# Performance work log

Hardware: AMD Instinct MI355X
Metric: run time of the kernel (lower is better)

## Reference

```python
import jax, jax.numpy as jnp
import numpy as np
from jax import lax

NUM_HEADS = 8
EPS = 1e-12  # torch F.normalize default eps


def setup_inputs() -> dict:
    key = jax.random.key(0)
    ks = jax.random.split(key, 7)
    B, C, H, W = 4, 128, 256, 256
    d = C // 2  # per-branch channels = 64
    x = jax.random.normal(ks[0], (B, C, H, W), jnp.float32)
    w_qkv1 = jax.random.normal(ks[1], (3 * d, d), jnp.float32) * 0.05
    w_qkv2 = jax.random.normal(ks[2], (3 * d, d), jnp.float32) * 0.05
    w_dw1 = jax.random.normal(ks[3], (3 * d, 1, 3, 3), jnp.float32) * 0.05
    w_dw2 = jax.random.normal(ks[4], (3 * d, 1, 3, 3), jnp.float32) * 0.05
    w_po1 = jax.random.normal(ks[5], (d, d), jnp.float32) * 0.05
    w_po2 = jax.random.normal(ks[6], (d, d), jnp.float32) * 0.05
    t1 = jnp.ones((NUM_HEADS, 1, 1), jnp.float32)
    t2 = jnp.ones((NUM_HEADS, 1, 1), jnp.float32)
    return {"x": x, "w_qkv1": w_qkv1, "w_qkv2": w_qkv2, "w_dw1": w_dw1,
            "w_dw2": w_dw2, "w_po1": w_po1, "w_po2": w_po2, "t1": t1, "t2": t2}


def _qkv(xb, w1x1, wdw):
    # 1x1 conv (pointwise) then 3x3 depthwise conv, no bias
    y = jnp.einsum('bchw,oc->bohw', xb, w1x1)
    y = lax.conv_general_dilated(
        y, wdw, window_strides=(1, 1), padding='SAME',
        dimension_numbers=('NCHW', 'OIHW', 'NCHW'),
        feature_group_count=y.shape[1])
    return y


def _heads(t, b, h, w):
    # b (head c) h w -> b head c (h*w)
    return t.reshape(b, NUM_HEADS, -1, h * w)


def _l2norm(t):
    n = jnp.sqrt(jnp.sum(t * t, axis=-1, keepdims=True))
    return t / jnp.maximum(n, EPS)


def reference(x, w_qkv1, w_qkv2, w_dw1, w_dw2, w_po1, w_po2, t1, t2):
    b, c, h, w = x.shape
    x1, x2 = jnp.split(x, 2, axis=1)
    q1, k1, v1 = jnp.split(_qkv(x1, w_qkv1, w_dw1), 3, axis=1)
    q2, k2, v2 = jnp.split(_qkv(x2, w_qkv2, w_dw2), 3, axis=1)
    q1, k1, v1 = (_heads(t, b, h, w) for t in (q1, k1, v1))
    q2, k2, v2 = (_heads(t, b, h, w) for t in (q2, k2, v2))
    q1, k1 = _l2norm(q1), _l2norm(k1)
    q2, k2 = _l2norm(q2), _l2norm(k2)
    # channel-wise attention: [b, head, c_h, c_h]
    attn1 = jax.nn.softmax(jnp.einsum('bhcn,bhdn->bhcd', q1, k1) * t1[None], axis=-1)
    attn2 = jax.nn.softmax(jnp.einsum('bhcn,bhdn->bhcd', q2, k2) * t2[None], axis=-1)
    # cross-branch V swap
    out1 = jnp.einsum('bhcd,bhdn->bhcn', attn1, v2).reshape(b, c // 2, h, w)
    out2 = jnp.einsum('bhcd,bhdn->bhcn', attn2, v1).reshape(b, c // 2, h, w)
    out1 = jnp.einsum('bchw,oc->bohw', out1, w_po1)
    out2 = jnp.einsum('bchw,oc->bohw', out2, w_po2)
    return jnp.concatenate([out1, out2], axis=1)
```

## Files before the change

### kernel.cpp

```cpp
#include <hip/hip_runtime.h>
#include <hip/hip_fp16.h>

#define NPIX 65536
#define WIMG 256
#define HIMG 256
#define TW 16
#define TH 8
#define HSTR 24
#define NSLOT 240
#define YCH 248

typedef __attribute__((ext_vector_type(8))) _Float16 half8;
typedef __attribute__((ext_vector_type(4))) float f32x4;

__device__ __forceinline__ unsigned int h2u(__half2 h) {
  union { __half2 h; unsigned int u; } c; c.h = h; return c.u;
}
__device__ __forceinline__ __half2 u2h(unsigned int u) {
  union { unsigned int u; __half2 h; } c; c.u = u; return c.h;
}
__device__ __forceinline__ __half2 sp2(_Float16 s) {
  union { _Float16 h[2]; __half2 v; } u; u.h[0] = s; u.h[1] = s; return u.v;
}
__device__ __forceinline__ int qk_idx(int ch, int pxblk) {
  return ch * 128 + ((pxblk ^ (ch & 7)) << 3);
}
__device__ __forceinline__ void ld16_lds(const void* g, void* l) {
  __builtin_amdgcn_global_load_lds(
      (const __attribute__((address_space(1))) unsigned int*)g,
      (__attribute__((address_space(3))) unsigned int*)l, 16, 0, 0);
}

__global__ __launch_bounds__(256)
void k_prep(const float* __restrict__ wq1, const float* __restrict__ wq2,
            const float* __restrict__ wd1, const float* __restrict__ wd2,
            float* __restrict__ zbuf,
            _Float16* __restrict__ wqh, _Float16* __restrict__ wdh) {
  int i = blockIdx.x * 256 + threadIdx.x;
  if (i < 6144) {
    zbuf[i] = 0.0f;
  } else {
    int j = i - 6144;
    if (j < 24576) {
      int br = j / 12288, r = j - br * 12288;
      wqh[j] = (_Float16)((br ? wq2 : wq1)[r]);
    } else {
      int k = j - 24576;
      int br = k / 3072, r = k - br * 3072;
      int o = r >> 4, t = r & 15;
      wdh[k] = (t < 9) ? (_Float16)((br ? wd2 : wd1)[o * 9 + t]) : (_Float16)0.0f;
    }
  }
}

__global__ __launch_bounds__(256)
void k_xt(const float* __restrict__ x, __half* __restrict__ xT) {
  __shared__ _Float16 tile[64 * 257];
  const int strip = blockIdx.x;
  const int br = blockIdx.y, b = blockIdx.z;
  const int tid = threadIdx.x;
  const float* xb = x + ((size_t)b * 128 + br * 64) * NPIX + strip * 256;
  #pragma unroll 8
  for (int c = 0; c < 64; ++c)
    tile[c * 257 + tid] = (_Float16)xb[(size_t)c * NPIX + tid];
  __syncthreads();
  __half* xo = xT + ((size_t)(b * 2 + br) * NPIX + strip * 256) * 64;
  const int j = tid & 7;
  #pragma unroll
  for (int i = 0; i < 8; ++i) {
    int p = (tid >> 3) + i * 32;
    half8 h;
    #pragma unroll
    for (int k = 0; k < 8; ++k) h[k] = tile[(j * 8 + k) * 257 + p];
    *(half8*)((_Float16*)xo + p * 64 + j * 8) = h;
  }
}

__global__ __launch_bounds__(256, 3)
void k_qkv(const __half* __restrict__ xT,
           const _Float16* __restrict__ wqh, const _Float16* __restrict__ wdh,
           const float* __restrict__ zpage,
           __half* __restrict__ vbuf, float* __restrict__ gram,
           float* __restrict__ sqq, float* __restrict__ sqk)
{
  __shared__ __align__(16) _Float16 xs[256 * 64];
  __shared__ __align__(16) _Float16 ys[32 * YCH];

  const int tid = threadIdx.x;
  const int lane = tid & 63;
  const int wid = tid >> 6;
  const int tile = blockIdx.x;
  const int br = blockIdx.y;
  const int b = blockIdx.z;
  const int tx0 = (tile & 15) * TW;
  const int ty0 = (tile >> 4) * TH;

  const _Float16* wqb = wqh + br * 12288;
  const _Float16* wdb = wdh + br * 3072;
  const __half* xTimg = xT + (size_t)(b * 2 + br) * NPIX * 64;

  {
    const int j = lane & 7, pl = lane >> 3;
    for (int it = wid; it < 30; it += 4) {
      int s = it * 8;
      int slot = s + pl;
      int hy = slot / HSTR;
      int hx = slot - hy * HSTR;
      int gy = ty0 - 1 + hy, gx = tx0 - 1 + hx;
      bool valid = (hx < 18) && ((unsigned)gy < HIMG) && ((unsigned)gx < WIMG);
      const void* src = valid
        ? (const void*)((const _Float16*)xTimg + (size_t)(gy * WIMG + gx) * 64
                        + ((j ^ (slot & 7)) << 3))
        : (const void*)((const char*)zpage + lane * 16);
      ld16_lds(src, (void*)(xs + s * 64));
    }
  }
  asm volatile("s_waitcnt vmcnt(0)" ::: "memory");
  __syncthreads();

  const int col = lane & 15;
  const int qrow = lane >> 4;
  const int oo = tid >> 3;
  const int row = tid & 7;

  unsigned int qreg[2][8], kreg[2][8];

  #pragma unroll
  for (int p = 0; p < 3; ++p) {
    #pragma unroll
    for (int h = 0; h < 2; ++h) {
      half8 wf[2][2];
      #pragma unroll
      for (int nt = 0; nt < 2; ++nt)
        #pragma unroll
        for (int kc = 0; kc < 2; ++kc)
          wf[kc][nt] = *(const half8*)(wqb
              + (((p * 64 + h * 32 + nt * 16 + col) << 6) + kc * 32 + qrow * 8));

      for (int mt = wid; mt < 15; mt += 4) {
        int px = mt * 16 + col;
        half8 af0 = *(const half8*)(xs + px * 64 + (((qrow    ) ^ (px & 7)) << 3));
        half8 af1 = *(const half8*)(xs + px * 64 + (((4 + qrow) ^ (px & 7)) << 3));
        f32x4 a0 = {0,0,0,0}, a1 = {0,0,0,0};
        a0 = __builtin_amdgcn_mfma_f32_16x16x32_f16(af0, wf[0][0], a0, 0, 0, 0);
        a0 = __builtin_amdgcn_mfma_f32_16x16x32_f16(af1, wf[1][0], a0, 0, 0, 0);
        a1 = __builtin_amdgcn_mfma_f32_16x16x32_f16(af0, wf[0][1], a1, 0, 0, 0);
        a1 = __builtin_amdgcn_mfma_f32_16x16x32_f16(af1, wf[1][1], a1, 0, 0, 0);
        int pxd = mt * 16 + qrow * 4;
        __half2* d0 = (__half2*)(ys + (col     ) * YCH + pxd);
        __half2* d1 = (__half2*)(ys + (col + 16) * YCH + pxd);
        d0[0] = __floats2half2_rn(a0[0], a0[1]);
        d0[1] = __floats2half2_rn(a0[2], a0[3]);
        d1[0] = __floats2half2_rn(a1[0], a1[1]);
        d1[1] = __floats2half2_rn(a1[2], a1[3]);
      }
      __syncthreads();

      {
        const int o = h * 32 + oo;
        const _Float16* wdp = wdb + ((p * 64 + o) << 4);
        half8 wv = *(const half8*)wdp;
        _Float16 w8v = wdp[8];
        __half2 w2[9];
        #pragma unroll
        for (int j = 0; j < 8; ++j) w2[j] = sp2(wv[j]);
        w2[8] = sp2(w8v);
        __half2 a[8];
        #pragma unroll
        for (int k2 = 0; k2 < 8; ++k2) a[k2] = u2h(0u);
        #pragma unroll
        for (int ky = 0; ky < 3; ++ky) {
          const _Float16* rp = ys + oo * YCH + (row + ky) * HSTR;
          uint4 ra = *(const uint4*)rp;
          uint4 rb = *(const uint4*)(rp + 8);
          unsigned int rc = *(const unsigned int*)(rp + 16);
          unsigned int A[9] = {ra.x, ra.y, ra.z, ra.w, rb.x, rb.y, rb.z, rb.w, rc};
          #pragma unroll
          for (int k2 = 0; k2 < 8; ++k2) {
            unsigned int M = (A[k2] >> 16) | (A[k2 + 1] << 16);
            a[k2] = __hfma2(w2[ky * 3 + 0], u2h(A[k2]), a[k2]);
            a[k2] = __hfma2(w2[ky * 3 + 1], u2h(M), a[k2]);
            a[k2] = __hfma2(w2[ky * 3 + 2], u2h(A[k2 + 1]), a[k2]);
          }
        }
        if (p == 0) {
          #pragma unroll
          for (int k2 = 0; k2 < 8; ++k2) qreg[h][k2] = h2u(a[k2]);
        } else if (p == 1) {
          #pragma unroll
          for (int k2 = 0; k2 < 8; ++k2) kreg[h][k2] = h2u(a[k2]);
        } else {
          __half* vrow = (__half*)(vbuf
              + ((size_t)((br * 4 + b) * 64 + o)) * NPIX
              + (ty0 + row) * WIMG + tx0);
          uint4 s0 = {h2u(a[0]), h2u(a[1]), h2u(a[2]), h2u(a[3])};
          uint4 s1 = {h2u(a[4]), h2u(a[5]), h2u(a[6]), h2u(a[7])};
          *(uint4*)vrow = s0;
          *(uint4*)(vrow + 8) = s1;
          if (h == 1) {
            _Float16* qsb = xs;
            _Float16* ksb = xs + 64 * 128;
            #pragma unroll
            for (int hh = 0; hh < 2; ++hh) {
              int ch = hh * 32 + oo;
              uint4 q0 = {qreg[hh][0], qreg[hh][1], qreg[hh][2], qreg[hh][3]};
              uint4 q1 = {qreg[hh][4], qreg[hh][5], qreg[hh][6], qreg[hh][7]};
              uint4 k0 = {kreg[hh][0], kreg[hh][1], kreg[hh][2], kreg[hh][3]};
              uint4 k1 = {kreg[hh][4], kreg[hh][5], kreg[hh][6], kreg[hh][7]};
              *(uint4*)(qsb + qk_idx(ch, 2 * row))     = q0;
              *(uint4*)(qsb + qk_idx(ch, 2 * row + 1)) = q1;
              *(uint4*)(ksb + qk_idx(ch, 2 * row))     = k0;
              *(uint4*)(ksb + qk_idx(ch, 2 * row + 1)) = k1;
            }
          }
        }
      }
      __syncthreads();
    }
  }

  {
    const _Float16* qsb = xs;
    const _Float16* ksb = xs + 64 * 128;
    f32x4 gqk = {0,0,0,0}, gqq = {0,0,0,0}, gkk = {0,0,0,0};
    int ch = wid * 16 + col;
    #pragma unroll
    for (int kc = 0; kc < 4; ++kc) {
      int pb = kc * 4 + qrow;
      half8 aq = *(const half8*)(qsb + qk_idx(ch, pb));
      half8 bk = *(const half8*)(ksb + qk_idx(ch, pb));
      gqk = __builtin_amdgcn_mfma_f32_16x16x32_f16(aq, bk, gqk, 0, 0, 0);
      gqq = __builtin_amdgcn_mfma_f32_16x16x32_f16(aq, aq, gqq, 0, 0, 0);
      gkk = __builtin_amdgcn_mfma_f32_16x16x32_f16(bk, bk, gkk, 0, 0, 0);
    }
    const int gb_off = (br * 4 + b);
    if (((lane >> 3) & 1) == (lane >> 5)) {
      float* gb = gram + gb_off * 512;
      int kch = ch;
      int qc0 = wid * 16 + qrow * 4;
      #pragma unroll
      for (int r = 0; r < 4; ++r) {
        int qch = qc0 + r;
        atomicAdd(&gb[(qch >> 3) * 64 + (qch & 7) * 8 + (kch & 7)], gqk[r]);
      }
    }
    if ((col >> 2) == qrow) {
      atomicAdd(&sqq[gb_off * 64 + ch], gqq[lane & 3]);
      atomicAdd(&sqk[gb_off * 64 + ch], gkk[lane & 3]);
    }
  }
}

__global__ __launch_bounds__(64)
void k_attn(const float* __restrict__ gram, const float* __restrict__ sqq,
            const float* __restrict__ sqk,
            const float* __restrict__ wpo1, const float* __restrict__ wpo2,
            const float* __restrict__ t1, const float* __restrict__ t2,
            _Float16* __restrict__ wefft)
{
  const int br = blockIdx.x, b = blockIdx.y;
  const int t = threadIdx.x;
  __shared__ float attn[8][8][8];
  const float* gb = gram + (br * 4 + b) * 512;
  const float* sq = sqq + (br * 4 + b) * 64;
  const float* sk = sqk + (br * 4 + b) * 64;
  const float* tt = br ? t2 : t1;
  {
    int h = t >> 3, cq = t & 7;
    float ts = tt[h];
    float qn = fmaxf(sqrtf(sq[h * 8 + cq]), 1e-12f);
    float lg[8], m = -1e30f;
    #pragma unroll
    for (int d2 = 0; d2 < 8; ++d2) {
      float kn = fmaxf(sqrtf(sk[h * 8 + d2]), 1e-12f);
      lg[d2] = ts * gb[h * 64 + cq * 8 + d2] / (qn * kn);
      m = fmaxf(m, lg[d2]);
    }
    float s = 0.f;
    #pragma unroll
    for (int d2 = 0; d2 < 8; ++d2) { lg[d2] = expf(lg[d2] - m); s += lg[d2]; }
    float inv = 1.0f / s;
    #pragma unroll
    for (int d2 = 0; d2 < 8; ++d2) attn[h][cq][d2] = lg[d2] * inv;
  }
  __syncthreads();
  const float* wpo = br ? wpo2 : wpo1;
  _Float16* wt = wefft + (br * 4 + b) * 4096;
  for (int cp = 0; cp < 64; ++cp) {
    int hp = cp >> 3, ip = cp & 7;
    float acc = 0.f;
    #pragma unroll
    for (int j = 0; j < 8; ++j)
      acc += wpo[t * 64 + hp * 8 + j] * attn[hp][j][ip];
    wt[t * 64 + cp] = (_Float16)acc;
  }
}

__global__ __launch_bounds__(256)
void k_out(const __half* __restrict__ vbuf, const _Float16* __restrict__ wefft,
           float* __restrict__ out)
{
  __shared__ __align__(16) _Float16 vs[64 * 128];
  __shared__ __align__(16) _Float16 vt[128 * 64];

  const int strip = blockIdx.x;
  const int obr = blockIdx.y, b = blockIdx.z;
  const int brv = 1 - obr;
  const int tid = threadIdx.x;
  const int lane = tid & 63;
  const int wid = tid >> 6;
  const int col = lane & 15;
  const int qrow = lane >> 4;

  const __half* vb = vbuf + ((size_t)(brv * 4 + b) * 64) * NPIX + strip * 128;

  for (int i = 0; i < 4; ++i) {
    int it = wid * 4 + i;
    const void* src = (const void*)((const _Float16*)vb
        + (size_t)(it * 4 + (lane >> 4)) * NPIX + (lane & 15) * 8);
    ld16_lds(src, (void*)(vs + it * 512));
  }
  asm volatile("s_waitcnt vmcnt(0)" ::: "memory");
  __syncthreads();

  {
    int px = tid & 127, cb = tid >> 7;
    #pragma unroll
    for (int j = 0; j < 4; ++j) {
      half8 h;
      #pragma unroll
      for (int e = 0; e < 8; ++e) h[e] = vs[(cb * 32 + j * 8 + e) * 128 + px];
      int chunk = cb * 4 + j;
      *(half8*)(vt + ((px * 8 + (chunk ^ (px & 7))) << 3)) = h;
    }
  }
  __syncthreads();

  const _Float16* wt = wefft + (obr * 4 + b) * 4096;
  half8 bf[2][4];
  #pragma unroll
  for (int nt = 0; nt < 4; ++nt)
    #pragma unroll
    for (int kc = 0; kc < 2; ++kc)
      bf[kc][nt] = *(const half8*)(wt + (nt * 16 + col) * 64 + kc * 32 + qrow * 8);

  float* ob = out + ((size_t)b * 128 + obr * 64) * NPIX + strip * 128;
  #pragma unroll
  for (int mi = 0; mi < 2; ++mi) {
    int mt = wid * 2 + mi;
    int px = mt * 16 + col;
    half8 af0 = *(const half8*)(vt + ((px * 8 + ((qrow    ) ^ (px & 7))) << 3));
    half8 af1 = *(const half8*)(vt + ((px * 8 + ((4 + qrow) ^ (px & 7))) << 3));
    f32x4 acc[4] = {{0,0,0,0},{0,0,0,0},{0,0,0,0},{0,0,0,0}};
    #pragma unroll
    for (int nt = 0; nt < 4; ++nt) {
      acc[nt] = __builtin_amdgcn_mfma_f32_16x16x32_f16(af0, bf[0][nt], acc[nt], 0, 0, 0);
      acc[nt] = __builtin_amdgcn_mfma_f32_16x16x32_f16(af1, bf[1][nt], acc[nt], 0, 0, 0);
    }
    int pxd = mt * 16 + qrow * 4;
    #pragma unroll
    for (int nt = 0; nt < 4; ++nt) {
      float4 s = {acc[nt][0], acc[nt][1], acc[nt][2], acc[nt][3]};
      *(float4*)(ob + (size_t)(nt * 16 + col) * NPIX + pxd) = s;
    }
  }
}

extern "C" void kernel_launch(void* const* d_in, const int* in_sizes, int n_in,
                              void* d_out, int out_size, void* d_ws, size_t ws_size,
                              hipStream_t stream) {
  const float* x     = (const float*)d_in[0];
  const float* wqkv1 = (const float*)d_in[1];
  const float* wqkv2 = (const float*)d_in[2];
  const float* wdw1  = (const float*)d_in[3];
  const float* wdw2  = (const float*)d_in[4];
  const float* wpo1  = (const float*)d_in[5];
  const float* wpo2  = (const float*)d_in[6];
  const float* t1    = (const float*)d_in[7];
  const float* t2    = (const float*)d_in[8];

  char* ws = (char*)d_ws;
  __half* vbuf = (__half*)ws;
  float* gram  = (float*)(ws + 67108864);
  float* sqq   = gram + 4096;
  float* sqk   = sqq + 512;
  float* zpage = sqk + 512;
  _Float16* wqkvh = (_Float16*)(zpage + 1024);
  _Float16* wdwh  = wqkvh + 24576;
  _Float16* wefft = wdwh + 6144;

  __half* xT = (__half*)d_out;

  k_prep<<<dim3(144), dim3(256), 0, stream>>>(wqkv1, wqkv2, wdw1, wdw2,
                                              gram, wqkvh, wdwh);
  k_xt<<<dim3(256, 2, 4), dim3(256), 0, stream>>>(x, xT);
  k_qkv<<<dim3(512, 2, 4), dim3(256), 0, stream>>>(xT, wqkvh, wdwh,
                                                   zpage, vbuf, gram, sqq, sqk);
  k_attn<<<dim3(2, 4), dim3(64), 0, stream>>>(gram, sqq, sqk, wpo1, wpo2, t1, t2, wefft);
  k_out<<<dim3(512, 2, 4), dim3(256), 0, stream>>>(vbuf, wefft, (float*)d_out);
}
```

Baseline: 226.6 us.

## Give each wave its own halo rows in k_qkv to drop block barriers

Restructures the fused pointwise+depthwise stage so each wave computes the pointwise conv for its own 48-pixel halo region (two output rows plus halo) into a private LDS slice and then runs the depthwise conv on it. This removes the per-pass __syncthreads pairs, leaving two barriers around the Q/K staging. Halo rows are now recomputed redundantly by neighbouring waves, about 192 pointwise pixels versus 240. Channels are processed in 16-wide groups, and register state for q/k is reorganised.

Result: no change. 224.2 us (-1.1%).

```diff
diff --git a/kernel.cpp b/kernel.cpp
--- a/kernel.cpp
+++ b/kernel.cpp
@@ -8,7 +8,7 @@
 #define TH 8
 #define HSTR 24
 #define NSLOT 240
-#define YCH 248
+#define YSW 104
 
 typedef __attribute__((ext_vector_type(8))) _Float16 half8;
 typedef __attribute__((ext_vector_type(4))) float f32x4;
@@ -84,7 +84,7 @@
            float* __restrict__ sqq, float* __restrict__ sqk)
 {
   __shared__ __align__(16) _Float16 xs[256 * 64];
-  __shared__ __align__(16) _Float16 ys[32 * YCH];
+  __shared__ __align__(16) _Float16 ys[4 * 16 * YSW];
 
   const int tid = threadIdx.x;
   const int lane = tid & 63;
@@ -120,104 +120,95 @@
 
   const int col = lane & 15;
   const int qrow = lane >> 4;
-  const int oo = tid >> 3;
-  const int row = tid & 7;
-
-  unsigned int qreg[2][8], kreg[2][8];
-
-  #pragma unroll
-  for (int p = 0; p < 3; ++p) {
-    #pragma unroll
-    for (int h = 0; h < 2; ++h) {
-      half8 wf[2][2];
-      #pragma unroll
-      for (int nt = 0; nt < 2; ++nt)
-        #pragma unroll
-        for (int kc = 0; kc < 2; ++kc)
-          wf[kc][nt] = *(const half8*)(wqb
-              + (((p * 64 + h * 32 + nt * 16 + col) << 6) + kc * 32 + qrow * 8));
-
-      for (int mt = wid; mt < 15; mt += 4) {
-        int px = mt * 16 + col;
-        half8 af0 = *(const half8*)(xs + px * 64 + (((qrow    ) ^ (px & 7)) << 3));
-        half8 af1 = *(const half8*)(xs + px * 64 + (((4 + qrow) ^ (px & 7)) << 3));
-        f32x4 a0 = {0,0,0,0}, a1 = {0,0,0,0};
-        a0 = __builtin_amdgcn_mfma_f32_16x16x32_f16(af0, wf[0][0], a0, 0, 0, 0);
-        a0 = __builtin_amdgcn_mfma_f32_16x16x32_f16(af1, wf[1][0], a0, 0, 0, 0);
-        a1 = __builtin_amdgcn_mfma_f32_16x16x32_f16(af0, wf[0][1], a1, 0, 0, 0);
-        a1 = __builtin_amdgcn_mfma_f32_16x16x32_f16(af1, wf[1][1], a1, 0, 0, 0);
-        int pxd = mt * 16 + qrow * 4;
-        __half2* d0 = (__half2*)(ys + (col     ) * YCH + pxd);
-        __half2* d1 = (__half2*)(ys + (col + 16) * YCH + pxd);
-        d0[0] = __floats2half2_rn(a0[0], a0[1]);
-        d0[1] = __floats2half2_rn(a0[2], a0[3]);
-        d1[0] = __floats2half2_rn(a1[0], a1[1]);
-        d1[1] = __floats2half2_rn(a1[2], a1[3]);
-      }
-      __syncthreads();
-
-      {
-        const int o = h * 32 + oo;
-        const _Float16* wdp = wdb + ((p * 64 + o) << 4);
-        half8 wv = *(const half8*)wdp;
-        _Float16 w8v = wdp[8];
-        __half2 w2[9];
-        #pragma unroll
-        for (int j = 0; j < 8; ++j) w2[j] = sp2(wv[j]);
-        w2[8] = sp2(w8v);
-        __half2 a[8];
-        #pragma unroll
-        for (int k2 = 0; k2 < 8; ++k2) a[k2] = u2h(0u);
-        #pragma unroll
-        for (int ky = 0; ky < 3; ++ky) {
-          const _Float16* rp = ys + oo * YCH + (row + ky) * HSTR;
-          uint4 ra = *(const uint4*)rp;
-          uint4 rb = *(const uint4*)(rp + 8);
-          unsigned int rc = *(const unsigned int*)(rp + 16);
-          unsigned int A[9] = {ra.x, ra.y, ra.z, ra.w, rb.x, rb.y, rb.z, rb.w, rc};
-          #pragma unroll
-          for (int k2 = 0; k2 < 8; ++k2) {
-            unsigned int M = (A[k2] >> 16) | (A[k2 + 1] << 16);
-            a[k2] = __hfma2(w2[ky * 3 + 0], u2h(A[k2]), a[k2]);
-            a[k2] = __hfma2(w2[ky * 3 + 1], u2h(M), a[k2]);
-            a[k2] = __hfma2(w2[ky * 3 + 2], u2h(A[k2 + 1]), a[k2]);
-          }
-        }
-        if (p == 0) {
-          #pragma unroll
-          for (int k2 = 0; k2 < 8; ++k2) qreg[h][k2] = h2u(a[k2]);
-        } else if (p == 1) {
-          #pragma unroll
-          for (int k2 = 0; k2 < 8; ++k2) kreg[h][k2] = h2u(a[k2]);
-        } else {
-          __half* vrow = (__half*)(vbuf
-              + ((size_t)((br * 4 + b) * 64 + o)) * NPIX
-              + (ty0 + row) * WIMG + tx0);
-          uint4 s0 = {h2u(a[0]), h2u(a[1]), h2u(a[2]), h2u(a[3])};
-          uint4 s1 = {h2u(a[4]), h2u(a[5]), h2u(a[6]), h2u(a[7])};
-          *(uint4*)vrow = s0;
-          *(uint4*)(vrow + 8) = s1;
-          if (h == 1) {
-            _Float16* qsb = xs;
-            _Float16* ksb = xs + 64 * 128;
-            #pragma unroll
-            for (int hh = 0; hh < 2; ++hh) {
-              int ch = hh * 32 + oo;
-              uint4 q0 = {qreg[hh][0], qreg[hh][1], qreg[hh][2], qreg[hh][3]};
-              uint4 q1 = {qreg[hh][4], qreg[hh][5], qreg[hh][6], qreg[hh][7]};
-              uint4 k0 = {kreg[hh][0], kreg[hh][1], kreg[hh][2], kreg[hh][3]};
-              uint4 k1 = {kreg[hh][4], kreg[hh][5], kreg[hh][6], kreg[hh][7]};
-              *(uint4*)(qsb + qk_idx(ch, 2 * row))     = q0;
-              *(uint4*)(qsb + qk_idx(ch, 2 * row + 1)) = q1;
-              *(uint4*)(ksb + qk_idx(ch, 2 * row))     = k0;
-              *(uint4*)(ksb + qk_idx(ch, 2 * row + 1)) = k1;
-            }
-          }
-        }
-      }
-      __syncthreads();
-    }
-  }
+  const int dc = lane >> 2;
+  const int rr = (lane >> 1) & 1;
+  const int dhalf = lane & 1;
+
+  _Float16* ysw = ys + wid * (16 * YSW);
+  unsigned int qreg[4][4], kreg[4][4];
+
+#define PW16(P_, G_) do {                                                     \
+    const _Float16* wp_ = wqb + ((((P_) * 64 + (G_) * 16 + col) << 6) + qrow * 8); \
+    half8 wf0_ = *(const half8*)(wp_);                                        \
+    half8 wf1_ = *(const half8*)(wp_ + 32);                                   \
+    _Pragma("unroll")                                                         \
+    for (int j = 0; j < 6; ++j) {                                             \
+      int px = wid * 48 + j * 16 + col;                                       \
+      half8 af0 = *(const half8*)(xs + px * 64 + (((qrow    ) ^ (px & 7)) << 3)); \
+      half8 af1 = *(const half8*)(xs + px * 64 + (((4 + qrow) ^ (px & 7)) << 3)); \
+      f32x4 a0 = {0,0,0,0};                                                   \
+      a0 = __builtin_amdgcn_mfma_f32_16x16x32_f16(af0, wf0_, a0, 0, 0, 0);    \
+      a0 = __builtin_amdgcn_mfma_f32_16x16x32_f16(af1, wf1_, a0, 0, 0, 0);    \
+      uint2 s_ = {h2u(__floats2half2_rn(a0[0], a0[1])),                       \
+                  h2u(__floats2half2_rn(a0[2], a0[3]))};                      \
+      *(uint2*)(ysw + col * YSW + j * 16 + qrow * 4) = s_;                    \
+    }                                                                         \
+  } while (0)
+
+#define DW16(P_, G_) do {                                                     \
+    const int o_ = (G_) * 16 + dc;                                            \
+    const _Float16* wdp_ = wdb + (((P_) * 64 + o_) << 4);                     \
+    half8 wv_ = *(const half8*)wdp_;                                          \
+    _Float16 w8_ = wdp_[8];                                                   \
+    __half2 w2_[9];                                                           \
+    _Pragma("unroll")                                                         \
+    for (int j = 0; j < 8; ++j) w2_[j] = sp2(wv_[j]);                         \
+    w2_[8] = sp2(w8_);                                                        \
+    __half2 a_[4];                                                            \
+    _Pragma("unroll")                                                         \
+    for (int k2 = 0; k2 < 4; ++k2) a_[k2] = u2h(0u);                          \
+    _Pragma("unroll")                                                         \
+    for (int ky = 0; ky < 3; ++ky) {                                          \
+      const _Float16* rp_ = ysw + dc * YSW + (rr + ky) * HSTR + dhalf * 8;    \
+      uint2 ra_ = *(const uint2*)rp_;                                         \
+      uint2 rb_ = *(const uint2*)(rp_ + 4);                                   \
+      unsigned int rc_ = *(const unsigned int*)(rp_ + 8);                     \
+      unsigned int W_[5] = {ra_.x, ra_.y, rb_.x, rb_.y, rc_};                 \
+      _Pragma("unroll")                                                       \
+      for (int k2 = 0; k2 < 4; ++k2) {                                        \
+        unsigned int M_ = (W_[k2] >> 16) | (W_[k2 + 1] << 16);                \
+        a_[k2] = __hfma2(w2_[ky * 3 + 0], u2h(W_[k2]), a_[k2]);               \
+        a_[k2] = __hfma2(w2_[ky * 3 + 1], u2h(M_), a_[k2]);                   \
+        a_[k2] = __hfma2(w2_[ky * 3 + 2], u2h(W_[k2 + 1]), a_[k2]);           \
+      }                                                                       \
+    }                                                                         \
+    if ((P_) == 0) {                                                          \
+      _Pragma("unroll")                                                       \
+      for (int k2 = 0; k2 < 4; ++k2) qreg[G_][k2] = h2u(a_[k2]);              \
+    } else if ((P_) == 1) {                                                   \
+      _Pragma("unroll")                                                       \
+      for (int k2 = 0; k2 < 4; ++k2) kreg[G_][k2] = h2u(a_[k2]);              \
+    } else {                                                                  \
+      __half* vrow_ = (__half*)(vbuf                                          \
+          + ((size_t)((br * 4 + b) * 64 + o_)) * NPIX                         \
+          + (ty0 + wid * 2 + rr) * WIMG + tx0 + dhalf * 8);                   \
+      uint4 s_ = {h2u(a_[0]), h2u(a_[1]), h2u(a_[2]), h2u(a_[3])};            \
+      *(uint4*)vrow_ = s_;                                                    \
+    }                                                                         \
+  } while (0)
+
+  PW16(2, 0); DW16(2, 0); PW16(2, 1); DW16(2, 1);
+  PW16(2, 2); DW16(2, 2); PW16(2, 3); DW16(2, 3);
+  PW16(0, 0); DW16(0, 0); PW16(0, 1); DW16(0, 1);
+  PW16(0, 2); DW16(0, 2); PW16(0, 3); DW16(0, 3);
+  PW16(1, 0); DW16(1, 0); PW16(1, 1); DW16(1, 1);
+  PW16(1, 2); DW16(1, 2); PW16(1, 3); DW16(1, 3);
+
+  __syncthreads();
+  {
+    _Float16* qsb = xs;
+    _Float16* ksb = xs + 64 * 128;
+    const int pb = wid * 4 + rr * 2 + dhalf;
+    #pragma unroll
+    for (int g = 0; g < 4; ++g) {
+      int ch = g * 16 + dc;
+      uint4 q_ = {qreg[g][0], qreg[g][1], qreg[g][2], qreg[g][3]};
+      uint4 k_ = {kreg[g][0], kreg[g][1], kreg[g][2], kreg[g][3]};
+      *(uint4*)(qsb + qk_idx(ch, pb)) = q_;
+      *(uint4*)(ksb + qk_idx(ch, pb)) = k_;
+    }
+  }
+  __syncthreads();
 
   {
     const _Float16* qsb = xs;
@@ -249,6 +240,8 @@
       atomicAdd(&sqk[gb_off * 64 + ch], gkk[lane & 3]);
     }
   }
+#undef PW16
+#undef DW16
 }
 
 __global__ __launch_bounds__(64)
```

## Fuse fp32-to-fp16 transpose into QKV kernel tile load, drop k_xt

Applied to the files above, without the earlier changes.

Removes the separate k_xt pass that converted x to a channel-last fp16 buffer, and instead has k_qkv read fp32 NCHW x directly, converting and swizzling into LDS during the halo tile load. This removes one full write and re-read of the intermediate transposed buffer plus a kernel launch. In exchange the loads are scalar strided 4-byte reads across channel planes (each halo pixel reads 64 channel planes), and halo pixels are re-read by neighboring tiles at fp32 width. The async direct-to-LDS loads are replaced by register-staged loads.

New measurement: 284.1 us. 1.25x slower.

```diff
diff --git a/kernel.cpp b/kernel.cpp
--- a/kernel.cpp
+++ b/kernel.cpp
@@ -53,33 +53,9 @@
   }
 }
 
-__global__ __launch_bounds__(256)
-void k_xt(const float* __restrict__ x, __half* __restrict__ xT) {
-  __shared__ _Float16 tile[64 * 257];
-  const int strip = blockIdx.x;
-  const int br = blockIdx.y, b = blockIdx.z;
-  const int tid = threadIdx.x;
-  const float* xb = x + ((size_t)b * 128 + br * 64) * NPIX + strip * 256;
-  #pragma unroll 8
-  for (int c = 0; c < 64; ++c)
-    tile[c * 257 + tid] = (_Float16)xb[(size_t)c * NPIX + tid];
-  __syncthreads();
-  __half* xo = xT + ((size_t)(b * 2 + br) * NPIX + strip * 256) * 64;
-  const int j = tid & 7;
-  #pragma unroll
-  for (int i = 0; i < 8; ++i) {
-    int p = (tid >> 3) + i * 32;
-    half8 h;
-    #pragma unroll
-    for (int k = 0; k < 8; ++k) h[k] = tile[(j * 8 + k) * 257 + p];
-    *(half8*)((_Float16*)xo + p * 64 + j * 8) = h;
-  }
-}
-
 __global__ __launch_bounds__(256, 3)
-void k_qkv(const __half* __restrict__ xT,
+void k_qkv(const float* __restrict__ x,
            const _Float16* __restrict__ wqh, const _Float16* __restrict__ wdh,
-           const float* __restrict__ zpage,
            __half* __restrict__ vbuf, float* __restrict__ gram,
            float* __restrict__ sqq, float* __restrict__ sqk)
 {
@@ -97,25 +73,30 @@
 
   const _Float16* wqb = wqh + br * 12288;
   const _Float16* wdb = wdh + br * 3072;
-  const __half* xTimg = xT + (size_t)(b * 2 + br) * NPIX * 64;
+  const float* xb = x + ((size_t)b * 128 + br * 64) * NPIX;
 
   {
-    const int j = lane & 7, pl = lane >> 3;
-    for (int it = wid; it < 30; it += 4) {
-      int s = it * 8;
-      int slot = s + pl;
-      int hy = slot / HSTR;
-      int hx = slot - hy * HSTR;
-      int gy = ty0 - 1 + hy, gx = tx0 - 1 + hx;
-      bool valid = (hx < 18) && ((unsigned)gy < HIMG) && ((unsigned)gx < WIMG);
-      const void* src = valid
-        ? (const void*)((const _Float16*)xTimg + (size_t)(gy * WIMG + gx) * 64
-                        + ((j ^ (slot & 7)) << 3))
-        : (const void*)((const char*)zpage + lane * 16);
-      ld16_lds(src, (void*)(xs + s * 64));
-    }
-  }
-  asm volatile("s_waitcnt vmcnt(0)" ::: "memory");
+    const int schunk = lane & 7, srow = lane >> 3;
+    #pragma unroll
+    for (int i = 0; i < 8; ++i) {
+      int s = (i * 4 + wid) * 8 + srow;
+      if (s < NSLOT) {
+        int hy = s / HSTR, hx = s - hy * HSTR;
+        int gy = ty0 - 1 + hy, gx = tx0 - 1 + hx;
+        bool valid = (hx < 18) && ((unsigned)gy < HIMG) && ((unsigned)gx < WIMG);
+        int gyc = min(max(gy, 0), HIMG - 1);
+        int gxc = min(max(gx, 0), WIMG - 1);
+        const float* xp = xb + (size_t)(schunk * 8) * NPIX + gyc * WIMG + gxc;
+        half8 h;
+        #pragma unroll
+        for (int e = 0; e < 8; ++e) {
+          float v = xp[(size_t)e * NPIX];
+          h[e] = valid ? (_Float16)v : (_Float16)0.0f;
+        }
+        *(half8*)(xs + s * 64 + ((schunk ^ srow) << 3)) = h;
+      }
+    }
+  }
   __syncthreads();
 
   const int col = lane & 15;
@@ -384,18 +365,15 @@
   float* gram  = (float*)(ws + 67108864);
   float* sqq   = gram + 4096;
   float* sqk   = sqq + 512;
-  float* zpage = sqk + 512;
-  _Float16* wqkvh = (_Float16*)(zpage + 1024);
+  float* zpad  = sqk + 512;
+  _Float16* wqkvh = (_Float16*)(zpad + 1024);
   _Float16* wdwh  = wqkvh + 24576;
   _Float16* wefft = wdwh + 6144;
 
-  __half* xT = (__half*)d_out;
-
   k_prep<<<dim3(144), dim3(256), 0, stream>>>(wqkv1, wqkv2, wdw1, wdw2,
                                               gram, wqkvh, wdwh);
-  k_xt<<<dim3(256, 2, 4), dim3(256), 0, stream>>>(x, xT);
-  k_qkv<<<dim3(512, 2, 4), dim3(256), 0, stream>>>(xT, wqkvh, wdwh,
-                                                   zpage, vbuf, gram, sqq, sqk);
+  k_qkv<<<dim3(512, 2, 4), dim3(256), 0, stream>>>(x, wqkvh, wdwh,
+                                                   vbuf, gram, sqq, sqk);
   k_attn<<<dim3(2, 4), dim3(64), 0, stream>>>(gram, sqq, sqk, wpo1, wpo2, t1, t2, wefft);
   k_out<<<dim3(512, 2, 4), dim3(256), 0, stream>>>(vbuf, wefft, (float*)d_out);
 }
```
